# Kernel tuning notes

Hardware: AMD Instinct MI355X
Metric: run time of the kernel (lower is better)

## Reference

```python
import jax, jax.numpy as jnp
import numpy as np

N, C_IN, C_OUT, J = 4096, 256, 256, 2
ATT_SLICE = C_OUT * J  # 512
DENSITY = 0.01
NEG_FILL = -1e20


def _sparse_lap(key, n):
    k1, k2 = jax.random.split(key)
    vals = jax.random.normal(k1, (n, n), dtype=jnp.float32)
    mask = jax.random.uniform(k2, (n, n)) < DENSITY
    return vals * mask + jnp.eye(n, dtype=jnp.float32)


def setup_inputs() -> dict:
    key = jax.random.key(0)
    ks = jax.random.split(key, 12)
    s = 0.05
    return {
        "x": jax.random.normal(ks[0], (N, C_IN), dtype=jnp.float32),
        "Lup": _sparse_lap(ks[1], N),
        "Ld": _sparse_lap(ks[2], N),
        "P": _sparse_lap(ks[3], N),
        "Wirr_w": jax.random.normal(ks[4], (J, C_OUT, C_IN), dtype=jnp.float32) * s,
        "Wirr_b": jax.random.normal(ks[5], (J, C_OUT), dtype=jnp.float32) * s,
        "Wsol_w": jax.random.normal(ks[6], (J, C_OUT, C_IN), dtype=jnp.float32) * s,
        "Wsol_b": jax.random.normal(ks[7], (J, C_OUT), dtype=jnp.float32) * s,
        "Whar_w": jax.random.normal(ks[8], (C_OUT, C_IN), dtype=jnp.float32) * s,
        "Whar_b": jax.random.normal(ks[9], (C_OUT,), dtype=jnp.float32) * s,
        "att_irr": jax.random.normal(ks[10], (2 * ATT_SLICE, 1), dtype=jnp.float32) * s,
        "att_sol": jax.random.normal(ks[11], (2 * ATT_SLICE, 1), dtype=jnp.float32) * s,
    }


def _branch(x, L, Ww, Wb, att):
    # x_cat = concat_j(Linear_j(x)) : [N, J*C_OUT]
    x_cat = (jnp.einsum('nc,jdc->njd', x, Ww) + Wb).reshape(x.shape[0], -1)
    src = x_cat @ att[:ATT_SLICE, :]   # [N,1]
    dst = x_cat @ att[ATT_SLICE:, :]   # [N,1]
    E = jax.nn.leaky_relu(src + dst.T, negative_slope=0.01)  # [N,N]
    E = jnp.where(L != 0, E, NEG_FILL)
    alpha = jax.nn.softmax(E, axis=-1)
    z = (alpha @ x) @ Ww[0].T + Wb[0]
    for p in range(1, J):  # Laplacian-power diffusion
        alpha = alpha @ L
        z = z + (alpha @ x) @ Ww[p].T + Wb[p]
    return z


def reference(x, Lup, Ld, P, Wirr_w, Wirr_b, Wsol_w, Wsol_b, Whar_w, Whar_b, att_irr, att_sol):
    z_i = _branch(x, Ld, Wirr_w, Wirr_b, att_irr)
    z_s = _branch(x, Lup, Wsol_w, Wsol_b, att_sol)
    z_har = (P @ x) @ Whar_w.T + Whar_b
    return z_i + z_s + z_har
```

## Files before the change

kernel.cpp:

```cpp
#include <hip/hip_runtime.h>

#define NROW 4096
#define CH   256
#define MAXNNZ 128

typedef short  short8  __attribute__((ext_vector_type(8)));
typedef unsigned short ushort8 __attribute__((ext_vector_type(8)));
typedef float  f32x4   __attribute__((ext_vector_type(4)));

__device__ inline unsigned short f2bf(float f) {
  unsigned u = __float_as_uint(f);
  return (unsigned short)((u + 0x7fffu + ((u >> 16) & 1u)) >> 16);
}
__device__ inline float bf2f(unsigned short h) {
  return __uint_as_float((unsigned)h << 16);
}
__device__ inline int mbcnt64(unsigned long long m, int base) {
  int t = __builtin_amdgcn_mbcnt_lo((unsigned)m, (unsigned)base);
  return __builtin_amdgcn_mbcnt_hi((unsigned)(m >> 32), t);
}

__global__ __launch_bounds__(256) void build_csr3(
    const float* __restrict__ L0, const float* __restrict__ L1,
    const float* __restrict__ L2, int* __restrict__ idx,
    float* __restrict__ val, int* __restrict__ cnt) {
  __shared__ int   sj[4][MAXNNZ];
  __shared__ float sv[4][MAXNNZ];
  const float* L = (blockIdx.y == 0) ? L0 : (blockIdx.y == 1) ? L1 : L2;
  int wi   = threadIdx.x >> 6;
  int row  = blockIdx.x * 4 + wi;
  int lane = threadIdx.x & 63;
  const float4* Lrow = (const float4*)(L + (size_t)row * NROW);

  float4 v[16];
#pragma unroll
  for (int k = 0; k < 16; ++k) v[k] = Lrow[k * 64 + lane];
  __builtin_amdgcn_sched_barrier(0);

  int base = 0;
#pragma unroll
  for (int k = 0; k < 16; ++k) {
    float4 q = v[k];
    bool n0 = q.x != 0.f, n1 = q.y != 0.f, n2 = q.z != 0.f, n3 = q.w != 0.f;
    unsigned long long b0 = __ballot(n0), b1 = __ballot(n1);
    unsigned long long b2 = __ballot(n2), b3 = __ballot(n3);
    int off = mbcnt64(b3, mbcnt64(b2, mbcnt64(b1, mbcnt64(b0, base))));
    int col0 = k * 256 + lane * 4;
    if (n0) { if (off < MAXNNZ) { sj[wi][off] = col0;     sv[wi][off] = q.x; } ++off; }
    if (n1) { if (off < MAXNNZ) { sj[wi][off] = col0 + 1; sv[wi][off] = q.y; } ++off; }
    if (n2) { if (off < MAXNNZ) { sj[wi][off] = col0 + 2; sv[wi][off] = q.z; } ++off; }
    if (n3) { if (off < MAXNNZ) { sj[wi][off] = col0 + 3; sv[wi][off] = q.w; } ++off; }
    base += __popcll(b0) + __popcll(b1) + __popcll(b2) + __popcll(b3);
  }

  size_t rbase = ((size_t)blockIdx.y * NROW + row) * MAXNNZ;
  int2   ji = ((const int2*)sj[wi])[lane];
  float2 vf = ((const float2*)sv[wi])[lane];
  ((int2*)(idx + rbase))[lane] = ji;
  ((float2*)(val + rbase))[lane] = vf;
  if (lane == 0) cnt[blockIdx.y * NROW + row] = base < MAXNNZ ? base : MAXNNZ;
}

__global__ void fold_att(const float* __restrict__ Wi, const float* __restrict__ bi,
                         const float* __restrict__ ai,
                         const float* __restrict__ Ws, const float* __restrict__ bs,
                         const float* __restrict__ as_,
                         float* __restrict__ wfold, float* __restrict__ bfold) {
  int b  = blockIdx.x >> 1;
  int sd = blockIdx.x & 1;
  const float* Ww  = b ? Ws : Wi;
  const float* Wb  = b ? bs : bi;
  const float* att = (b ? as_ : ai) + sd * 512;
  int c = threadIdx.x;
  float acc = 0.f;
  for (int k = 0; k < 512; ++k) acc += att[k] * Ww[k * 256 + c];
  wfold[blockIdx.x * 256 + c] = acc;
  __shared__ float sb[256];
  sb[c] = att[c] * Wb[c] + att[c + 256] * Wb[c + 256];
  __syncthreads();
  for (int s2 = 128; s2 > 0; s2 >>= 1) { if (c < s2) sb[c] += sb[c + s2]; __syncthreads(); }
  if (c == 0) bfold[blockIdx.x] = sb[0];
}

__global__ void src_dst(const float* __restrict__ x, const float* __restrict__ wfold,
                        const float* __restrict__ bfold, float* __restrict__ sdv) {
  int q    = blockIdx.y;
  int row  = blockIdx.x * 4 + (threadIdx.x >> 6);
  int lane = threadIdx.x & 63;
  const float4* xr = (const float4*)(x + (size_t)row * CH);
  const float4* wr = (const float4*)(wfold + q * CH);
  float4 a = xr[lane];
  float4 b = wr[lane];
  float s = a.x * b.x + a.y * b.y + a.z * b.z + a.w * b.w;
  for (int o = 32; o; o >>= 1) s += __shfl_xor(s, o);
  if (lane == 0) sdv[q * NROW + row] = s + bfold[q];
}

__global__ void cvt_all(const float* __restrict__ x, const float* __restrict__ Wi,
                        const float* __restrict__ Ws, const float* __restrict__ Wh,
                        unsigned short* __restrict__ xbf, unsigned short* __restrict__ Bbf) {
  int i = blockIdx.x * 256 + threadIdx.x;
  const float* src; unsigned short* dst; int o;
  if (i < 262144)        { src = x;  dst = xbf;          o = i; }
  else if (i < 294912)   { src = Wi; dst = Bbf;          o = i - 262144; }
  else if (i < 327680)   { src = Ws; dst = Bbf + 131072; o = i - 294912; }
  else                   { src = Wh; dst = Bbf + 262144; o = i - 327680; }
  float4 v = ((const float4*)src)[o];
  ushort4 u;
  u.x = f2bf(v.x); u.y = f2bf(v.y); u.z = f2bf(v.z); u.w = f2bf(v.w);
  ((ushort4*)dst)[o] = u;
}

__global__ __launch_bounds__(256, 2) void gemm_mfma(const unsigned short* __restrict__ A,
                                                    const unsigned short* __restrict__ Bt,
                                                    unsigned short* __restrict__ Y) {
  __shared__ unsigned short sA[64 * 256];
  __shared__ unsigned short sB[64 * 256];
  const int m0 = blockIdx.x * 64, n0 = blockIdx.y * 64;
  const int tid = threadIdx.x, wid = tid >> 6, lane = tid & 63;

  for (int c = 0; c < 8; ++c) {
    int chunk = c * 256 + tid;
    int r  = chunk >> 5;
    int cb = (chunk & 31) * 16;
    int cbs = cb ^ ((r & 7) << 4);
    ushort8 va = *(const ushort8*)((const char*)(A  + (size_t)(m0 + r) * 256) + cb);
    *(ushort8*)((char*)sA + r * 512 + cbs) = va;
    ushort8 vb = *(const ushort8*)((const char*)(Bt + (size_t)(n0 + r) * 256) + cb);
    *(ushort8*)((char*)sB + r * 512 + cbs) = vb;
  }
  __syncthreads();

  const int wr = wid >> 1, wc = wid & 1;
  const int lr = lane & 15, kg = lane >> 4;
  f32x4 acc[2][2] = {};
#pragma unroll
  for (int ks = 0; ks < 8; ++ks) {
    int kb = ks * 64 + kg * 16;
    short8 a0, a1, b0, b1;
    { int r = wr * 32 + lr;      a0 = *(const short8*)((const char*)sA + r * 512 + (kb ^ ((r & 7) << 4))); }
    { int r = wr * 32 + 16 + lr; a1 = *(const short8*)((const char*)sA + r * 512 + (kb ^ ((r & 7) << 4))); }
    { int r = wc * 32 + lr;      b0 = *(const short8*)((const char*)sB + r * 512 + (kb ^ ((r & 7) << 4))); }
    { int r = wc * 32 + 16 + lr; b1 = *(const short8*)((const char*)sB + r * 512 + (kb ^ ((r & 7) << 4))); }
    acc[0][0] = __builtin_amdgcn_mfma_f32_16x16x32_bf16(a0, b0, acc[0][0], 0, 0, 0);
    acc[0][1] = __builtin_amdgcn_mfma_f32_16x16x32_bf16(a0, b1, acc[0][1], 0, 0, 0);
    acc[1][0] = __builtin_amdgcn_mfma_f32_16x16x32_bf16(a1, b0, acc[1][0], 0, 0, 0);
    acc[1][1] = __builtin_amdgcn_mfma_f32_16x16x32_bf16(a1, b1, acc[1][1], 0, 0, 0);
  }

#pragma unroll
  for (int mi = 0; mi < 2; ++mi)
#pragma unroll
    for (int ni = 0; ni < 2; ++ni) {
      int col = n0 + wc * 32 + ni * 16 + lr;
#pragma unroll
      for (int r4 = 0; r4 < 4; ++r4) {
        int row = m0 + wr * 32 + mi * 16 + kg * 4 + r4;
        Y[(size_t)row * 1280 + col] = f2bf(acc[mi][ni][r4]);
      }
    }
}

__global__ void spmm_add(const int* __restrict__ idx, const float* __restrict__ val,
                         const int* __restrict__ cnt, unsigned short* __restrict__ Y) {
  int br = blockIdx.y;
  int row = blockIdx.x, t = threadIdx.x;
  size_t rbase = ((size_t)br * NROW + row) * MAXNNZ;
  int n = cnt[br * NROW + row];
  __shared__ int   sj[MAXNNZ];
  __shared__ float sv[MAXNNZ];
  if (t < n) { sj[t] = idx[rbase + t]; sv[t] = val[rbase + t]; }
  __syncthreads();
  int cs = br ? 768 : 256, cd = br ? 512 : 0;
  float acc = bf2f(Y[(size_t)row * 1280 + cd + t]);
  for (int k = 0; k < n; ++k) acc += sv[k] * bf2f(Y[(size_t)sj[k] * 1280 + cs + t]);
  Y[(size_t)row * 1280 + cd + t] = f2bf(acc);
}

__global__ void final_z(const int* __restrict__ idx, const float* __restrict__ val,
                        const int* __restrict__ cnt, const float* __restrict__ sdv,
                        const unsigned short* __restrict__ Y,
                        const float* __restrict__ bi, const float* __restrict__ bs,
                        const float* __restrict__ bh, float* __restrict__ Z) {
  int row = blockIdx.x, t = threadIdx.x;
  __shared__ float sa[MAXNNZ];
  __shared__ int   sj[MAXNNZ];
  __shared__ float red[4];
  float acc = bi[t] + bi[256 + t] + bs[t] + bs[256 + t] + bh[t];

  for (int br = 0; br < 2; ++br) {
    size_t rbase = ((size_t)br * NROW + row) * MAXNNZ;
    int n = cnt[br * NROW + row];
    const float* srcv = sdv + (2 * br) * NROW;
    const float* dstv = sdv + (2 * br + 1) * NROW;
    float e = -1e30f;
    if (t < n) {
      int j = idx[rbase + t];
      sj[t] = j;
      float v = srcv[row] + dstv[j];
      e = v >= 0.f ? v : 0.01f * v;
    }
    float m = e;
    for (int o = 32; o; o >>= 1) m = fmaxf(m, __shfl_xor(m, o));
    if ((t & 63) == 0) red[t >> 6] = m;
    __syncthreads();
    m = fmaxf(fmaxf(red[0], red[1]), fmaxf(red[2], red[3]));
    __syncthreads();
    float p = (t < n) ? expf(e - m) : 0.f;
    float s = p;
    for (int o = 32; o; o >>= 1) s += __shfl_xor(s, o);
    if ((t & 63) == 0) red[t >> 6] = s;
    __syncthreads();
    s = red[0] + red[1] + red[2] + red[3];
    if (t < n) sa[t] = p / s;
    __syncthreads();
    int cd = br ? 512 : 0;
    for (int k = 0; k < n; ++k)
      acc += sa[k] * bf2f(Y[(size_t)sj[k] * 1280 + cd + t]);
    __syncthreads();
  }

  {
    size_t rbase = ((size_t)2 * NROW + row) * MAXNNZ;
    int n = cnt[2 * NROW + row];
    if (t < n) { sj[t] = idx[rbase + t]; sa[t] = val[rbase + t]; }
    __syncthreads();
    for (int k = 0; k < n; ++k)
      acc += sa[k] * bf2f(Y[(size_t)sj[k] * 1280 + 1024 + t]);
  }
  Z[(size_t)row * 256 + t] = acc;
}

extern "C" void kernel_launch(void* const* d_in, const int* in_sizes, int n_in,
                              void* d_out, int out_size, void* d_ws, size_t ws_size,
                              hipStream_t stream) {
  const float* x      = (const float*)d_in[0];
  const float* Lup    = (const float*)d_in[1];
  const float* Ld     = (const float*)d_in[2];
  const float* P      = (const float*)d_in[3];
  const float* Wirr_w = (const float*)d_in[4];
  const float* Wirr_b = (const float*)d_in[5];
  const float* Wsol_w = (const float*)d_in[6];
  const float* Wsol_b = (const float*)d_in[7];
  const float* Whar_w = (const float*)d_in[8];
  const float* Whar_b = (const float*)d_in[9];
  const float* att_i  = (const float*)d_in[10];
  const float* att_s  = (const float*)d_in[11];
  float* Z = (float*)d_out;

  char* w = (char*)d_ws;
  auto alloc = [&](size_t bytes) { void* p = (void*)w; w += (bytes + 255) & ~(size_t)255; return p; };

  int*   idx  = (int*)alloc((size_t)3 * NROW * MAXNNZ * 4);
  float* val  = (float*)alloc((size_t)3 * NROW * MAXNNZ * 4);
  int*   cnt  = (int*)alloc((size_t)3 * NROW * 4);
  float* wfold = (float*)alloc(4 * CH * 4);
  float* bfold = (float*)alloc(4 * 4);
  float* sdv   = (float*)alloc(4 * NROW * 4);
  unsigned short* xbf = (unsigned short*)alloc((size_t)NROW * CH * 2);
  unsigned short* Bbf = (unsigned short*)alloc((size_t)1280 * CH * 2);
  unsigned short* Y   = (unsigned short*)alloc((size_t)NROW * 1280 * 2);

  build_csr3<<<dim3(NROW / 4, 3), 256, 0, stream>>>(Ld, Lup, P, idx, val, cnt);

  fold_att<<<4, 256, 0, stream>>>(Wirr_w, Wirr_b, att_i, Wsol_w, Wsol_b, att_s, wfold, bfold);
  src_dst<<<dim3(NROW / 4, 4), 256, 0, stream>>>(x, wfold, bfold, sdv);

  cvt_all<<<(262144 + 32768 + 32768 + 16384) / 256, 256, 0, stream>>>(x, Wirr_w, Wsol_w, Whar_w, xbf, Bbf);

  gemm_mfma<<<dim3(NROW / 64, 1280 / 64), 256, 0, stream>>>(xbf, Bbf, Y);

  spmm_add<<<dim3(NROW, 2), 256, 0, stream>>>(idx, val, cnt, Y);

  final_z<<<NROW, 256, 0, stream>>>(idx, val, cnt, sdv, Y, Wirr_b, Wsol_b, Whar_b, Z);
}
```

Measured before the change: 130.5 us.

## Build sparse rows as quarter-row segments with persistent prefetching grid

The dense-to-sparse conversion now splits each Laplacian row into four 1024-column segments, each handled by one wave. A fixed grid of 2048 blocks loops over six segment batches and prefetches the next batch's loads while compacting the current one. Each segment is stored as packed (column, value) int2 pairs with up to 40 slots, and consumer kernels merge the four segments into LDS when they stage a row. The goal is to hide memory latency in the 200MB dense read and to cut CSR output size. The cost is a per-segment cap of 40 nonzeros, where the old per-row cap was 128.

```diff
diff --git a/kernel.cpp b/kernel.cpp
--- a/kernel.cpp
+++ b/kernel.cpp
@@ -2,7 +2,8 @@
 
 #define NROW 4096
 #define CH   256
-#define MAXNNZ 128
+#define SEGSLOT 40
+#define LDSNNZ  160
 
 typedef short  short8  __attribute__((ext_vector_type(8)));
 typedef unsigned short ushort8 __attribute__((ext_vector_type(8)));
@@ -20,45 +21,60 @@
   return __builtin_amdgcn_mbcnt_hi((unsigned)(m >> 32), t);
 }
 
-__global__ __launch_bounds__(256) void build_csr3(
+__global__ __launch_bounds__(256) void seg_csr(
     const float* __restrict__ L0, const float* __restrict__ L1,
-    const float* __restrict__ L2, int* __restrict__ idx,
-    float* __restrict__ val, int* __restrict__ cnt) {
-  __shared__ int   sj[4][MAXNNZ];
-  __shared__ float sv[4][MAXNNZ];
-  const float* L = (blockIdx.y == 0) ? L0 : (blockIdx.y == 1) ? L1 : L2;
-  int wi   = threadIdx.x >> 6;
-  int row  = blockIdx.x * 4 + wi;
-  int lane = threadIdx.x & 63;
-  const float4* Lrow = (const float4*)(L + (size_t)row * NROW);
-
-  float4 v[16];
-#pragma unroll
-  for (int k = 0; k < 16; ++k) v[k] = Lrow[k * 64 + lane];
-  __builtin_amdgcn_sched_barrier(0);
-
-  int base = 0;
-#pragma unroll
-  for (int k = 0; k < 16; ++k) {
-    float4 q = v[k];
-    bool n0 = q.x != 0.f, n1 = q.y != 0.f, n2 = q.z != 0.f, n3 = q.w != 0.f;
-    unsigned long long b0 = __ballot(n0), b1 = __ballot(n1);
-    unsigned long long b2 = __ballot(n2), b3 = __ballot(n3);
-    int off = mbcnt64(b3, mbcnt64(b2, mbcnt64(b1, mbcnt64(b0, base))));
-    int col0 = k * 256 + lane * 4;
-    if (n0) { if (off < MAXNNZ) { sj[wi][off] = col0;     sv[wi][off] = q.x; } ++off; }
-    if (n1) { if (off < MAXNNZ) { sj[wi][off] = col0 + 1; sv[wi][off] = q.y; } ++off; }
-    if (n2) { if (off < MAXNNZ) { sj[wi][off] = col0 + 2; sv[wi][off] = q.z; } ++off; }
-    if (n3) { if (off < MAXNNZ) { sj[wi][off] = col0 + 3; sv[wi][off] = q.w; } ++off; }
-    base += __popcll(b0) + __popcll(b1) + __popcll(b2) + __popcll(b3);
-  }
-
-  size_t rbase = ((size_t)blockIdx.y * NROW + row) * MAXNNZ;
-  int2   ji = ((const int2*)sj[wi])[lane];
-  float2 vf = ((const float2*)sv[wi])[lane];
-  ((int2*)(idx + rbase))[lane] = ji;
-  ((float2*)(val + rbase))[lane] = vf;
-  if (lane == 0) cnt[blockIdx.y * NROW + row] = base < MAXNNZ ? base : MAXNNZ;
+    const float* __restrict__ L2, int2* __restrict__ segout,
+    int* __restrict__ segcnt) {
+  __shared__ int2 sbuf[4][SEGSLOT];
+  const int wi = threadIdx.x >> 6, lane = threadIdx.x & 63;
+  const int NW = 8192;
+  int u = blockIdx.x * 4 + wi;
+
+  auto addr = [&](int uu) -> const float4* {
+    int mat = uu >> 14;
+    const float* Lm = (mat == 0) ? L0 : (mat == 1) ? L1 : L2;
+    return (const float4*)(Lm + ((size_t)((uu >> 2) & 4095) << 12) + ((uu & 3) << 10));
+  };
+
+  float4 c0, c1, c2, c3;
+  { const float4* p = addr(u); c0 = p[lane]; c1 = p[64 + lane]; c2 = p[128 + lane]; c3 = p[192 + lane]; }
+
+#pragma unroll 1
+  for (int it = 0; it < 6; ++it) {
+    float4 x0, x1, x2, x3;
+    if (it < 5) {
+      const float4* p = addr(u + NW);
+      x0 = p[lane]; x1 = p[64 + lane]; x2 = p[128 + lane]; x3 = p[192 + lane];
+    }
+    __builtin_amdgcn_sched_barrier(0);
+
+    int base = 0;
+    int colbase = (u & 3) * 1024 + lane * 4;
+#define PROCQ(q, cb) {                                                          \
+    bool a0 = q.x != 0.f, a1 = q.y != 0.f, a2 = q.z != 0.f, a3 = q.w != 0.f;    \
+    unsigned long long b0 = __ballot(a0), b1 = __ballot(a1);                    \
+    unsigned long long b2 = __ballot(a2), b3 = __ballot(a3);                    \
+    int off = mbcnt64(b3, mbcnt64(b2, mbcnt64(b1, mbcnt64(b0, base))));         \
+    if (a0) { if (off < SEGSLOT) sbuf[wi][off] = make_int2((cb),     __float_as_int(q.x)); ++off; } \
+    if (a1) { if (off < SEGSLOT) sbuf[wi][off] = make_int2((cb) + 1, __float_as_int(q.y)); ++off; } \
+    if (a2) { if (off < SEGSLOT) sbuf[wi][off] = make_int2((cb) + 2, __float_as_int(q.z)); ++off; } \
+    if (a3) { if (off < SEGSLOT) sbuf[wi][off] = make_int2((cb) + 3, __float_as_int(q.w)); ++off; } \
+    base += __popcll(b0) + __popcll(b1) + __popcll(b2) + __popcll(b3); }
+    PROCQ(c0, colbase)
+    PROCQ(c1, colbase + 256)
+    PROCQ(c2, colbase + 512)
+    PROCQ(c3, colbase + 768)
+#undef PROCQ
+
+    int2 e;
+    if (lane < SEGSLOT) e = sbuf[wi][lane];
+    int2* outp = segout + (size_t)u * SEGSLOT;
+    if (lane < SEGSLOT) outp[lane] = e;
+    if (lane == 0) segcnt[u] = base < SEGSLOT ? base : SEGSLOT;
+
+    c0 = x0; c1 = x1; c2 = x2; c3 = x3;
+    u += NW;
+  }
 }
 
 __global__ void fold_att(const float* __restrict__ Wi, const float* __restrict__ bi,
@@ -161,15 +177,30 @@
     }
 }
 
-__global__ void spmm_add(const int* __restrict__ idx, const float* __restrict__ val,
-                         const int* __restrict__ cnt, unsigned short* __restrict__ Y) {
+__device__ inline int stage_row(const int2* __restrict__ segout,
+                                const int* __restrict__ segcnt, int mr, int t,
+                                int* sj, float* sv) {
+  int4 cn = ((const int4*)segcnt)[mr];
+  int c0 = cn.x, p1 = c0 + cn.y, p2 = p1 + cn.z, tot = p2 + cn.w;
+  if (t < tot) {
+    int s, o;
+    if      (t < c0) { s = 0; o = t; }
+    else if (t < p1) { s = 1; o = t - c0; }
+    else if (t < p2) { s = 2; o = t - p1; }
+    else             { s = 3; o = t - p2; }
+    int2 e = segout[((size_t)mr * 4 + s) * SEGSLOT + o];
+    sj[t] = e.x; sv[t] = __int_as_float(e.y);
+  }
+  return tot;
+}
+
+__global__ void spmm_add(const int2* __restrict__ segout, const int* __restrict__ segcnt,
+                         unsigned short* __restrict__ Y) {
   int br = blockIdx.y;
   int row = blockIdx.x, t = threadIdx.x;
-  size_t rbase = ((size_t)br * NROW + row) * MAXNNZ;
-  int n = cnt[br * NROW + row];
-  __shared__ int   sj[MAXNNZ];
-  __shared__ float sv[MAXNNZ];
-  if (t < n) { sj[t] = idx[rbase + t]; sv[t] = val[rbase + t]; }
+  __shared__ int   sj[LDSNNZ];
+  __shared__ float sv[LDSNNZ];
+  int n = stage_row(segout, segcnt, br * NROW + row, t, sj, sv);
   __syncthreads();
   int cs = br ? 768 : 256, cd = br ? 512 : 0;
   float acc = bf2f(Y[(size_t)row * 1280 + cd + t]);
@@ -177,27 +208,25 @@
   Y[(size_t)row * 1280 + cd + t] = f2bf(acc);
 }
 
-__global__ void final_z(const int* __restrict__ idx, const float* __restrict__ val,
-                        const int* __restrict__ cnt, const float* __restrict__ sdv,
+__global__ void final_z(const int2* __restrict__ segout, const int* __restrict__ segcnt,
+                        const float* __restrict__ sdv,
                         const unsigned short* __restrict__ Y,
                         const float* __restrict__ bi, const float* __restrict__ bs,
                         const float* __restrict__ bh, float* __restrict__ Z) {
   int row = blockIdx.x, t = threadIdx.x;
-  __shared__ float sa[MAXNNZ];
-  __shared__ int   sj[MAXNNZ];
+  __shared__ float sa[LDSNNZ];
+  __shared__ int   sj[LDSNNZ];
   __shared__ float red[4];
   float acc = bi[t] + bi[256 + t] + bs[t] + bs[256 + t] + bh[t];
 
   for (int br = 0; br < 2; ++br) {
-    size_t rbase = ((size_t)br * NROW + row) * MAXNNZ;
-    int n = cnt[br * NROW + row];
+    int n = stage_row(segout, segcnt, br * NROW + row, t, sj, sa);
+    __syncthreads();
     const float* srcv = sdv + (2 * br) * NROW;
     const float* dstv = sdv + (2 * br + 1) * NROW;
     float e = -1e30f;
     if (t < n) {
-      int j = idx[rbase + t];
-      sj[t] = j;
-      float v = srcv[row] + dstv[j];
+      float v = srcv[row] + dstv[sj[t]];
       e = v >= 0.f ? v : 0.01f * v;
     }
     float m = e;
@@ -221,9 +250,7 @@
   }
 
   {
-    size_t rbase = ((size_t)2 * NROW + row) * MAXNNZ;
-    int n = cnt[2 * NROW + row];
-    if (t < n) { sj[t] = idx[rbase + t]; sa[t] = val[rbase + t]; }
+    int n = stage_row(segout, segcnt, 2 * NROW + row, t, sj, sa);
     __syncthreads();
     for (int k = 0; k < n; ++k)
       acc += sa[k] * bf2f(Y[(size_t)sj[k] * 1280 + 1024 + t]);
@@ -251,9 +278,8 @@
   char* w = (char*)d_ws;
   auto alloc = [&](size_t bytes) { void* p = (void*)w; w += (bytes + 255) & ~(size_t)255; return p; };
 
-  int*   idx  = (int*)alloc((size_t)3 * NROW * MAXNNZ * 4);
-  float* val  = (float*)alloc((size_t)3 * NROW * MAXNNZ * 4);
-  int*   cnt  = (int*)alloc((size_t)3 * NROW * 4);
+  int2* segout = (int2*)alloc((size_t)3 * NROW * 4 * SEGSLOT * 8);
+  int*  segcnt = (int*)alloc((size_t)3 * NROW * 4 * 4);
   float* wfold = (float*)alloc(4 * CH * 4);
   float* bfold = (float*)alloc(4 * 4);
   float* sdv   = (float*)alloc(4 * NROW * 4);
@@ -261,7 +287,7 @@
   unsigned short* Bbf = (unsigned short*)alloc((size_t)1280 * CH * 2);
   unsigned short* Y   = (unsigned short*)alloc((size_t)NROW * 1280 * 2);
 
-  build_csr3<<<dim3(NROW / 4, 3), 256, 0, stream>>>(Ld, Lup, P, idx, val, cnt);
+  seg_csr<<<2048, 256, 0, stream>>>(Ld, Lup, P, segout, segcnt);
 
   fold_att<<<4, 256, 0, stream>>>(Wirr_w, Wirr_b, att_i, Wsol_w, Wsol_b, att_s, wfold, bfold);
   src_dst<<<dim3(NROW / 4, 4), 256, 0, stream>>>(x, wfold, bfold, sdv);
@@ -270,7 +296,7 @@
 
   gemm_mfma<<<dim3(NROW / 64, 1280 / 64), 256, 0, stream>>>(xbf, Bbf, Y);
 
-  spmm_add<<<dim3(NROW, 2), 256, 0, stream>>>(idx, val, cnt, Y);
-
-  final_z<<<NROW, 256, 0, stream>>>(idx, val, cnt, sdv, Y, Wirr_b, Wsol_b, Whar_b, Z);
-}
+  spmm_add<<<dim3(NROW, 2), 256, 0, stream>>>(segout, segcnt, Y);
+
+  final_z<<<NROW, 256, 0, stream>>>(segout, segcnt, sdv, Y, Wirr_b, Wsol_b, Whar_b, Z);
+}
```

Result: no change. 131.8 us (+1.0%).

## Compute attention scores from GEMM output and vectorize sparse gathers across waves

Applied to the files above, without the earlier changes.

Drops the fold_att and src_dst kernels. Attention src/dst scores are now computed from the bf16 GEMM output Y in a new sdv_from_y kernel, and the biases are folded in. spmm_add and final_z now give each of the four waves its own subset of nonzeros, gather 4 bf16 values per lane with vector loads, and reduce the partial sums through shared memory. The aim is to cut kernel launches and to use wider, more parallel gathers. The cost is extra LDS traffic and scores computed from bf16-rounded Y rather than fp32 x.

```diff
diff --git a/kernel.cpp b/kernel.cpp
--- a/kernel.cpp
+++ b/kernel.cpp
@@ -20,80 +20,52 @@
   return __builtin_amdgcn_mbcnt_hi((unsigned)(m >> 32), t);
 }
 
-__global__ __launch_bounds__(256) void build_csr3(
+__global__ __launch_bounds__(256, 4) void build_csr3(
     const float* __restrict__ L0, const float* __restrict__ L1,
     const float* __restrict__ L2, int* __restrict__ idx,
     float* __restrict__ val, int* __restrict__ cnt) {
   __shared__ int   sj[4][MAXNNZ];
   __shared__ float sv[4][MAXNNZ];
-  const float* L = (blockIdx.y == 0) ? L0 : (blockIdx.y == 1) ? L1 : L2;
-  int wi   = threadIdx.x >> 6;
-  int row  = blockIdx.x * 4 + wi;
-  int lane = threadIdx.x & 63;
+  const int mat = blockIdx.y;
+  const float* L = (mat == 0) ? L0 : (mat == 1) ? L1 : L2;
+  const int wi = threadIdx.x >> 6, lane = threadIdx.x & 63;
+  const int row = blockIdx.x * 4 + wi;
   const float4* Lrow = (const float4*)(L + (size_t)row * NROW);
 
-  float4 v[16];
-#pragma unroll
-  for (int k = 0; k < 16; ++k) v[k] = Lrow[k * 64 + lane];
+  float4 v0  = Lrow[lane],        v1  = Lrow[64 + lane];
+  float4 v2  = Lrow[128 + lane],  v3  = Lrow[192 + lane];
+  float4 v4  = Lrow[256 + lane],  v5  = Lrow[320 + lane];
+  float4 v6  = Lrow[384 + lane],  v7  = Lrow[448 + lane];
+  float4 v8  = Lrow[512 + lane],  v9  = Lrow[576 + lane];
+  float4 v10 = Lrow[640 + lane],  v11 = Lrow[704 + lane];
+  float4 v12 = Lrow[768 + lane],  v13 = Lrow[832 + lane];
+  float4 v14 = Lrow[896 + lane],  v15 = Lrow[960 + lane];
   __builtin_amdgcn_sched_barrier(0);
 
   int base = 0;
-#pragma unroll
-  for (int k = 0; k < 16; ++k) {
-    float4 q = v[k];
-    bool n0 = q.x != 0.f, n1 = q.y != 0.f, n2 = q.z != 0.f, n3 = q.w != 0.f;
-    unsigned long long b0 = __ballot(n0), b1 = __ballot(n1);
-    unsigned long long b2 = __ballot(n2), b3 = __ballot(n3);
-    int off = mbcnt64(b3, mbcnt64(b2, mbcnt64(b1, mbcnt64(b0, base))));
-    int col0 = k * 256 + lane * 4;
-    if (n0) { if (off < MAXNNZ) { sj[wi][off] = col0;     sv[wi][off] = q.x; } ++off; }
-    if (n1) { if (off < MAXNNZ) { sj[wi][off] = col0 + 1; sv[wi][off] = q.y; } ++off; }
-    if (n2) { if (off < MAXNNZ) { sj[wi][off] = col0 + 2; sv[wi][off] = q.z; } ++off; }
-    if (n3) { if (off < MAXNNZ) { sj[wi][off] = col0 + 3; sv[wi][off] = q.w; } ++off; }
-    base += __popcll(b0) + __popcll(b1) + __popcll(b2) + __popcll(b3);
-  }
-
-  size_t rbase = ((size_t)blockIdx.y * NROW + row) * MAXNNZ;
+#define PROCQ(q, cb) {                                                         \
+    bool a0 = q.x != 0.f, a1 = q.y != 0.f, a2 = q.z != 0.f, a3 = q.w != 0.f;   \
+    unsigned long long b0 = __ballot(a0), b1 = __ballot(a1);                   \
+    unsigned long long b2 = __ballot(a2), b3 = __ballot(a3);                   \
+    int off = mbcnt64(b3, mbcnt64(b2, mbcnt64(b1, mbcnt64(b0, base))));        \
+    if (a0) { if (off < MAXNNZ) { sj[wi][off] = (cb);     sv[wi][off] = q.x; } ++off; } \
+    if (a1) { if (off < MAXNNZ) { sj[wi][off] = (cb) + 1; sv[wi][off] = q.y; } ++off; } \
+    if (a2) { if (off < MAXNNZ) { sj[wi][off] = (cb) + 2; sv[wi][off] = q.z; } ++off; } \
+    if (a3) { if (off < MAXNNZ) { sj[wi][off] = (cb) + 3; sv[wi][off] = q.w; } ++off; } \
+    base += __popcll(b0) + __popcll(b1) + __popcll(b2) + __popcll(b3); }
+  int cb = lane * 4;
+  PROCQ(v0,  cb)        PROCQ(v1,  cb + 256)  PROCQ(v2,  cb + 512)  PROCQ(v3,  cb + 768)
+  PROCQ(v4,  cb + 1024) PROCQ(v5,  cb + 1280) PROCQ(v6,  cb + 1536) PROCQ(v7,  cb + 1792)
+  PROCQ(v8,  cb + 2048) PROCQ(v9,  cb + 2304) PROCQ(v10, cb + 2560) PROCQ(v11, cb + 2816)
+  PROCQ(v12, cb + 3072) PROCQ(v13, cb + 3328) PROCQ(v14, cb + 3584) PROCQ(v15, cb + 3840)
+#undef PROCQ
+
+  size_t rbase = ((size_t)mat * NROW + row) * MAXNNZ;
   int2   ji = ((const int2*)sj[wi])[lane];
   float2 vf = ((const float2*)sv[wi])[lane];
   ((int2*)(idx + rbase))[lane] = ji;
   ((float2*)(val + rbase))[lane] = vf;
-  if (lane == 0) cnt[blockIdx.y * NROW + row] = base < MAXNNZ ? base : MAXNNZ;
-}
-
-__global__ void fold_att(const float* __restrict__ Wi, const float* __restrict__ bi,
-                         const float* __restrict__ ai,
-                         const float* __restrict__ Ws, const float* __restrict__ bs,
-                         const float* __restrict__ as_,
-                         float* __restrict__ wfold, float* __restrict__ bfold) {
-  int b  = blockIdx.x >> 1;
-  int sd = blockIdx.x & 1;
-  const float* Ww  = b ? Ws : Wi;
-  const float* Wb  = b ? bs : bi;
-  const float* att = (b ? as_ : ai) + sd * 512;
-  int c = threadIdx.x;
-  float acc = 0.f;
-  for (int k = 0; k < 512; ++k) acc += att[k] * Ww[k * 256 + c];
-  wfold[blockIdx.x * 256 + c] = acc;
-  __shared__ float sb[256];
-  sb[c] = att[c] * Wb[c] + att[c + 256] * Wb[c + 256];
-  __syncthreads();
-  for (int s2 = 128; s2 > 0; s2 >>= 1) { if (c < s2) sb[c] += sb[c + s2]; __syncthreads(); }
-  if (c == 0) bfold[blockIdx.x] = sb[0];
-}
-
-__global__ void src_dst(const float* __restrict__ x, const float* __restrict__ wfold,
-                        const float* __restrict__ bfold, float* __restrict__ sdv) {
-  int q    = blockIdx.y;
-  int row  = blockIdx.x * 4 + (threadIdx.x >> 6);
-  int lane = threadIdx.x & 63;
-  const float4* xr = (const float4*)(x + (size_t)row * CH);
-  const float4* wr = (const float4*)(wfold + q * CH);
-  float4 a = xr[lane];
-  float4 b = wr[lane];
-  float s = a.x * b.x + a.y * b.y + a.z * b.z + a.w * b.w;
-  for (int o = 32; o; o >>= 1) s += __shfl_xor(s, o);
-  if (lane == 0) sdv[q * NROW + row] = s + bfold[q];
+  if (lane == 0) cnt[mat * NROW + row] = base < MAXNNZ ? base : MAXNNZ;
 }
 
 __global__ void cvt_all(const float* __restrict__ x, const float* __restrict__ Wi,
@@ -161,32 +133,93 @@
     }
 }
 
-__global__ void spmm_add(const int* __restrict__ idx, const float* __restrict__ val,
-                         const int* __restrict__ cnt, unsigned short* __restrict__ Y) {
-  int br = blockIdx.y;
-  int row = blockIdx.x, t = threadIdx.x;
+__global__ __launch_bounds__(256) void sdv_from_y(
+    const unsigned short* __restrict__ Y, const float* __restrict__ ai,
+    const float* __restrict__ as_, const float* __restrict__ bi,
+    const float* __restrict__ bs, float* __restrict__ sdv) {
+  __shared__ float satt[2048];
+  __shared__ float sbias[4];
+  int t = threadIdx.x, wi = t >> 6, lane = t & 63;
+  for (int k = t; k < 1024; k += 256) { satt[k] = ai[k]; satt[1024 + k] = as_[k]; }
+  {
+    const float* av = (wi & 2) ? as_ : ai;
+    const float* bv = (wi & 2) ? bs : bi;
+    int off = (wi & 1) * 512;
+    float b = 0.f;
+    for (int k = lane; k < 512; k += 64) b += av[off + k] * bv[k];
+    for (int o = 32; o; o >>= 1) b += __shfl_xor(b, o);
+    if (lane == 0) sbias[wi] = b;
+  }
+  __syncthreads();
+
+  int row = blockIdx.x * 4 + wi;
+  const ushort8* yr = (const ushort8*)(Y + (size_t)row * 1280);
+  ushort8 ya = yr[lane * 2], yb = yr[lane * 2 + 1];
+  int c0 = lane * 16;
+  int off = (lane < 32) ? 0 : 512;
+  float a0 = 0.f, a1 = 0.f;
+#pragma unroll
+  for (int j = 0; j < 8; ++j) {
+    float y = bf2f(ya[j]); int c = c0 + j;
+    a0 += satt[off + c] * y; a1 += satt[off + 512 + c] * y;
+  }
+#pragma unroll
+  for (int j = 0; j < 8; ++j) {
+    float y = bf2f(yb[j]); int c = c0 + 8 + j;
+    a0 += satt[off + c] * y; a1 += satt[off + 512 + c] * y;
+  }
+  for (int o = 16; o; o >>= 1) { a0 += __shfl_xor(a0, o); a1 += __shfl_xor(a1, o); }
+  if (lane == 0)  { sdv[row] = a0 + sbias[0];            sdv[NROW + row] = a1 + sbias[1]; }
+  if (lane == 32) { sdv[2 * NROW + row] = a0 + sbias[2]; sdv[3 * NROW + row] = a1 + sbias[3]; }
+}
+
+__global__ __launch_bounds__(256) void spmm_add(const int* __restrict__ idx,
+                                                const float* __restrict__ val,
+                                                const int* __restrict__ cnt,
+                                                unsigned short* __restrict__ Y) {
+  int br = blockIdx.y, row = blockIdx.x;
+  int t = threadIdx.x, w = t >> 6, l = t & 63;
+  __shared__ int   sj[MAXNNZ];
+  __shared__ float sv[MAXNNZ];
+  __shared__ float part[4][256];
   size_t rbase = ((size_t)br * NROW + row) * MAXNNZ;
   int n = cnt[br * NROW + row];
-  __shared__ int   sj[MAXNNZ];
-  __shared__ float sv[MAXNNZ];
   if (t < n) { sj[t] = idx[rbase + t]; sv[t] = val[rbase + t]; }
   __syncthreads();
   int cs = br ? 768 : 256, cd = br ? 512 : 0;
-  float acc = bf2f(Y[(size_t)row * 1280 + cd + t]);
-  for (int k = 0; k < n; ++k) acc += sv[k] * bf2f(Y[(size_t)sj[k] * 1280 + cs + t]);
-  Y[(size_t)row * 1280 + cd + t] = f2bf(acc);
-}
-
-__global__ void final_z(const int* __restrict__ idx, const float* __restrict__ val,
-                        const int* __restrict__ cnt, const float* __restrict__ sdv,
+  float4 acc = {0.f, 0.f, 0.f, 0.f};
+  for (int k = w; k < n; k += 4) {
+    ushort4 y = *(const ushort4*)(Y + (size_t)sj[k] * 1280 + cs + 4 * l);
+    float a = sv[k];
+    acc.x += a * bf2f(y.x); acc.y += a * bf2f(y.y);
+    acc.z += a * bf2f(y.z); acc.w += a * bf2f(y.w);
+  }
+  ((float4*)part[w])[l] = acc;
+  __syncthreads();
+  if (t < 64) {
+    unsigned short* yp = Y + (size_t)row * 1280 + cd + 4 * t;
+    ushort4 yb = *(const ushort4*)yp;
+    ushort4 o;
+    o.x = f2bf(bf2f(yb.x) + part[0][4 * t]     + part[1][4 * t]     + part[2][4 * t]     + part[3][4 * t]);
+    o.y = f2bf(bf2f(yb.y) + part[0][4 * t + 1] + part[1][4 * t + 1] + part[2][4 * t + 1] + part[3][4 * t + 1]);
+    o.z = f2bf(bf2f(yb.z) + part[0][4 * t + 2] + part[1][4 * t + 2] + part[2][4 * t + 2] + part[3][4 * t + 2]);
+    o.w = f2bf(bf2f(yb.w) + part[0][4 * t + 3] + part[1][4 * t + 3] + part[2][4 * t + 3] + part[3][4 * t + 3]);
+    *(ushort4*)yp = o;
+  }
+}
+
+__global__ __launch_bounds__(256) void final_z(const int* __restrict__ idx,
+                        const float* __restrict__ val, const int* __restrict__ cnt,
+                        const float* __restrict__ sdv,
                         const unsigned short* __restrict__ Y,
                         const float* __restrict__ bi, const float* __restrict__ bs,
                         const float* __restrict__ bh, float* __restrict__ Z) {
-  int row = blockIdx.x, t = threadIdx.x;
+  int row = blockIdx.x, t = threadIdx.x, w = t >> 6, l = t & 63;
   __shared__ float sa[MAXNNZ];
   __shared__ int   sj[MAXNNZ];
   __shared__ float red[4];
-  float acc = bi[t] + bi[256 + t] + bs[t] + bs[256 + t] + bh[t];
+  __shared__ float part[4][256];
+  float4 acc = {0.f, 0.f, 0.f, 0.f};
 
   for (int br = 0; br < 2; ++br) {
     size_t rbase = ((size_t)br * NROW + row) * MAXNNZ;
@@ -215,8 +248,12 @@
     if (t < n) sa[t] = p / s;
     __syncthreads();
     int cd = br ? 512 : 0;
-    for (int k = 0; k < n; ++k)
-      acc += sa[k] * bf2f(Y[(size_t)sj[k] * 1280 + cd + t]);
+    for (int k = w; k < n; k += 4) {
+      ushort4 y = *(const ushort4*)(Y + (size_t)sj[k] * 1280 + cd + 4 * l);
+      float a = sa[k];
+      acc.x += a * bf2f(y.x); acc.y += a * bf2f(y.y);
+      acc.z += a * bf2f(y.z); acc.w += a * bf2f(y.w);
+    }
     __syncthreads();
   }
 
@@ -225,10 +262,24 @@
     int n = cnt[2 * NROW + row];
     if (t < n) { sj[t] = idx[rbase + t]; sa[t] = val[rbase + t]; }
     __syncthreads();
-    for (int k = 0; k < n; ++k)
-      acc += sa[k] * bf2f(Y[(size_t)sj[k] * 1280 + 1024 + t]);
-  }
-  Z[(size_t)row * 256 + t] = acc;
+    for (int k = w; k < n; k += 4) {
+      ushort4 y = *(const ushort4*)(Y + (size_t)sj[k] * 1280 + 1024 + 4 * l);
+      float a = sa[k];
+      acc.x += a * bf2f(y.x); acc.y += a * bf2f(y.y);
+      acc.z += a * bf2f(y.z); acc.w += a * bf2f(y.w);
+    }
+  }
+  ((float4*)part[w])[l] = acc;
+  __syncthreads();
+  if (t < 64) {
+    float4 r;
+    int c = 4 * t;
+    r.x = part[0][c]     + part[1][c]     + part[2][c]     + part[3][c]     + bi[c]     + bi[256 + c]     + bs[c]     + bs[256 + c]     + bh[c];
+    r.y = part[0][c + 1] + part[1][c + 1] + part[2][c + 1] + part[3][c + 1] + bi[c + 1] + bi[257 + c]     + bs[c + 1] + bs[257 + c]     + bh[c + 1];
+    r.z = part[0][c + 2] + part[1][c + 2] + part[2][c + 2] + part[3][c + 2] + bi[c + 2] + bi[258 + c]     + bs[c + 2] + bs[258 + c]     + bh[c + 2];
+    r.w = part[0][c + 3] + part[1][c + 3] + part[2][c + 3] + part[3][c + 3] + bi[c + 3] + bi[259 + c]     + bs[c + 3] + bs[259 + c]     + bh[c + 3];
+    *(float4*)(Z + (size_t)row * 256 + c) = r;
+  }
 }
 
 extern "C" void kernel_launch(void* const* d_in, const int* in_sizes, int n_in,
@@ -254,22 +305,19 @@
   int*   idx  = (int*)alloc((size_t)3 * NROW * MAXNNZ * 4);
   float* val  = (float*)alloc((size_t)3 * NROW * MAXNNZ * 4);
   int*   cnt  = (int*)alloc((size_t)3 * NROW * 4);
-  float* wfold = (float*)alloc(4 * CH * 4);
-  float* bfold = (float*)alloc(4 * 4);
-  float* sdv   = (float*)alloc(4 * NROW * 4);
+  float* sdv  = (float*)alloc(4 * NROW * 4);
   unsigned short* xbf = (unsigned short*)alloc((size_t)NROW * CH * 2);
   unsigned short* Bbf = (unsigned short*)alloc((size_t)1280 * CH * 2);
   unsigned short* Y   = (unsigned short*)alloc((size_t)NROW * 1280 * 2);
 
   build_csr3<<<dim3(NROW / 4, 3), 256, 0, stream>>>(Ld, Lup, P, idx, val, cnt);
 
-  fold_att<<<4, 256, 0, stream>>>(Wirr_w, Wirr_b, att_i, Wsol_w, Wsol_b, att_s, wfold, bfold);
-  src_dst<<<dim3(NROW / 4, 4), 256, 0, stream>>>(x, wfold, bfold, sdv);
-
   cvt_all<<<(262144 + 32768 + 32768 + 16384) / 256, 256, 0, stream>>>(x, Wirr_w, Wsol_w, Whar_w, xbf, Bbf);
 
   gemm_mfma<<<dim3(NROW / 64, 1280 / 64), 256, 0, stream>>>(xbf, Bbf, Y);
 
+  sdv_from_y<<<NROW / 4, 256, 0, stream>>>(Y, att_i, att_s, Wirr_b, Wsol_b, sdv);
+
   spmm_add<<<dim3(NROW, 2), 256, 0, stream>>>(idx, val, cnt, Y);
 
   final_z<<<NROW, 256, 0, stream>>>(idx, val, cnt, sdv, Y, Wirr_b, Wsol_b, Whar_b, Z);
```

Result: faster. 114.1 us (-12.6%).
